# Optimization experiments

Measured on AMD Instinct MI355X. Metric: run time of the kernel, lower is better.

## Reference

```python
import jax, jax.numpy as jnp
import numpy as np

B, S, H = 2, 2048, 1024
NH, DH = 16, 64  # num heads, head dim

def setup_inputs() -> dict:
    key = jax.random.key(0)
    ks = jax.random.split(key, 4)
    scale = 0.02
    return {
        "hidden_states": jax.random.normal(ks[0], (B, S, H), dtype=jnp.float32),
        "attention_mask": jnp.zeros((B, 1, 1, S), dtype=jnp.float32),  # additive mask
        "Wq": jax.random.normal(ks[1], (H, H), dtype=jnp.float32) * scale,
        "bq": jnp.zeros((H,), dtype=jnp.float32),
        "Wk": jax.random.normal(ks[2], (H, H), dtype=jnp.float32) * scale,
        "bk": jnp.zeros((H,), dtype=jnp.float32),
        "Wv": jax.random.normal(ks[3], (H, H), dtype=jnp.float32) * scale,
        "bv": jnp.zeros((H,), dtype=jnp.float32),
    }

def _split_heads(x):
    # [B,S,H] -> [B,NH,S,DH]
    return x.reshape(B, S, NH, DH).transpose(0, 2, 1, 3)

def reference(hidden_states, attention_mask, Wq, bq, Wk, bk, Wv, bv):
    q = _split_heads(hidden_states @ Wq + bq)
    k = _split_heads(hidden_states @ Wk + bk)
    v = _split_heads(hidden_states @ Wv + bv)
    # scores: [B,NH,S,S]
    scores = jnp.einsum('bhqd,bhkd->bhqk', q, k) / jnp.asarray(np.sqrt(DH), scores_dtype := q.dtype)
    scores = scores + attention_mask  # additive mask broadcast
    probs = jax.nn.softmax(scores, axis=-1)
    out = jnp.einsum('bhqk,bhkd->bhqd', probs, v)  # [B,NH,S,DH]
    out = out.transpose(0, 2, 1, 3).reshape(B, S, H)
    return out
```

## Files before the change

### kernel.cpp

```cpp
#include <hip/hip_runtime.h>
#include <hip/hip_bf16.h>

#define Bn  2
#define Sn  2048
#define Hn  1024
#define NHn 16
#define DHn 64
#define Mn  (Bn * Sn)

typedef __attribute__((ext_vector_type(4)))  float    f32x4;
typedef __attribute__((ext_vector_type(16))) float    f32x16;
typedef __attribute__((ext_vector_type(8)))  _Float16 h8;
typedef __attribute__((ext_vector_type(4)))  _Float16 h4;

#define MFMA16F(a, b, c) __builtin_amdgcn_mfma_f32_16x16x32_f16(a, b, c, 0, 0, 0)
#define MFMA32F(a, b, c) __builtin_amdgcn_mfma_f32_32x32x16_f16(a, b, c, 0, 0, 0)

__device__ __forceinline__ void glds16(const void* g, void* l) {
    __builtin_amdgcn_global_load_lds(
        (const __attribute__((address_space(1))) unsigned int*)g,
        (__attribute__((address_space(3))) unsigned int*)l, 16, 0, 0);
}

__global__ __launch_bounds__(256) void cvt_x(
    const float* __restrict__ X, _Float16* __restrict__ Xh)
{
    const int i = blockIdx.x * 256 + threadIdx.x;
    float4 x = ((const float4*)X)[i];
    h4 o;
    o[0] = (_Float16)x.x; o[1] = (_Float16)x.y;
    o[2] = (_Float16)x.z; o[3] = (_Float16)x.w;
    *(h4*)&Xh[(size_t)i * 4] = o;
}

__global__ __launch_bounds__(256) void cvt_wT(
    const float* __restrict__ W0, const float* __restrict__ W1,
    const float* __restrict__ W2, _Float16* __restrict__ WT)
{
    const int which = blockIdx.z;
    const float* W = (which == 0) ? W0 : (which == 1 ? W1 : W2);
    _Float16* O = WT + (size_t)which * Hn * Hn;

    const int k0 = blockIdx.x * 64;
    const int n0 = blockIdx.y * 64;
    const int tid = threadIdx.x;

    __shared__ float Ws[64][65];

#pragma unroll
    for (int it = 0; it < 4; ++it) {
        const int idx = tid + 256 * it;
        const int row = idx >> 4, c4 = (idx & 15) * 4;
        float4 w = *(const float4*)&W[(size_t)(k0 + row) * Hn + n0 + c4];
        Ws[row][c4 + 0] = w.x; Ws[row][c4 + 1] = w.y;
        Ws[row][c4 + 2] = w.z; Ws[row][c4 + 3] = w.w;
    }
    __syncthreads();
#pragma unroll
    for (int it = 0; it < 16; ++it) {
        const int e = tid + 256 * it;
        const int k = e & 63, n = e >> 6;
        O[(size_t)(n0 + n) * Hn + k0 + k] = (_Float16)Ws[k][n];
    }
}

__global__ __launch_bounds__(256) void qkv_mfma(
    const _Float16* __restrict__ Xh, const _Float16* __restrict__ WTA,
    const float* __restrict__ b0, const float* __restrict__ b1,
    const float* __restrict__ b2,
    _Float16* __restrict__ Qh, _Float16* __restrict__ Kh,
    _Float16* __restrict__ VTh)
{
    const int which = blockIdx.z;
    const _Float16* WT = WTA + (size_t)which * Hn * Hn;
    const float* bias = (which == 0) ? b0 : (which == 1 ? b1 : b2);
    _Float16* Dst = (which == 0) ? Qh : (which == 1 ? Kh : VTh);

    const int m0 = blockIdx.x * 128;
    const int n0 = blockIdx.y * 128;
    const int tid  = threadIdx.x;
    const int wid  = tid >> 6;
    const int lane = tid & 63;
    const int l16  = lane & 15;
    const int quad = lane >> 4;
    const int wm = wid >> 1, wn = wid & 1;

    __shared__ _Float16 Ah[128 * 32], Bh[128 * 32];

    f32x4 acc[4][4];
#pragma unroll
    for (int i = 0; i < 4; ++i)
#pragma unroll
        for (int j = 0; j < 4; ++j) acc[i][j] = (f32x4){0.f, 0.f, 0.f, 0.f};

    for (int kt = 0; kt < Hn / 32; ++kt) {
        const int k0 = kt * 32;
        __syncthreads();
#pragma unroll
        for (int c = 0; c < 2; ++c) {
            const int idx = (wid * 2 + c) * 64 + lane;
            const int row = idx >> 2;
            const int cg  = (idx & 3) ^ (row & 3);
            glds16(&Xh[(size_t)(m0 + row) * Hn + k0 + cg * 8],
                   &Ah[(wid * 2 + c) * 512]);
            glds16(&WT[(size_t)(n0 + row) * Hn + k0 + cg * 8],
                   &Bh[(wid * 2 + c) * 512]);
        }
        __syncthreads();

        h8 xa[4], wb[4];
#pragma unroll
        for (int t = 0; t < 4; ++t) {
            const int ar = wm * 64 + t * 16 + l16;
            const int br = wn * 64 + t * 16 + l16;
            xa[t] = *(const h8*)&Ah[ar * 32 + ((quad ^ (ar & 3)) * 8)];
            wb[t] = *(const h8*)&Bh[br * 32 + ((quad ^ (br & 3)) * 8)];
        }
        if (which < 2) {
#pragma unroll
            for (int i = 0; i < 4; ++i)
#pragma unroll
                for (int j = 0; j < 4; ++j)
                    acc[i][j] = MFMA16F(xa[i], wb[j], acc[i][j]);
        } else {
#pragma unroll
            for (int i = 0; i < 4; ++i)
#pragma unroll
                for (int j = 0; j < 4; ++j)
                    acc[i][j] = MFMA16F(wb[i], xa[j], acc[i][j]);
        }
    }

    if (which < 2) {
#pragma unroll
        for (int j = 0; j < 4; ++j) {
            const int n = n0 + wn * 64 + j * 16 + l16;
            const float bv = bias[n];
            const int hh = n >> 6, dd = n & 63;
#pragma unroll
            for (int i = 0; i < 4; ++i) {
                const int mb = m0 + wm * 64 + i * 16 + quad * 4;
#pragma unroll
                for (int r = 0; r < 4; ++r) {
                    const int m = mb + r;
                    const int b = m >> 11, s = m & (Sn - 1);
                    Dst[(((size_t)b * NHn + hh) * Sn + s) * DHn + dd] =
                        (_Float16)(acc[i][j][r] + bv);
                }
            }
        }
    } else {
#pragma unroll
        for (int i = 0; i < 4; ++i) {
#pragma unroll
            for (int r = 0; r < 4; ++r) {
                const int n = n0 + wn * 64 + i * 16 + quad * 4 + r;
                const float bv = bias[n];
                const int hh = n >> 6, dd = n & 63;
#pragma unroll
                for (int j = 0; j < 4; ++j) {
                    const int m = m0 + wm * 64 + j * 16 + l16;
                    const int b = m >> 11, s = m & (Sn - 1);
                    Dst[(((size_t)b * NHn + hh) * DHn + dd) * Sn + s] =
                        (_Float16)(acc[i][j][r] + bv);
                }
            }
        }
    }
}

__global__ __launch_bounds__(256) void attn(
    const _Float16* __restrict__ Qh, const _Float16* __restrict__ Kh,
    const _Float16* __restrict__ VTh, const float* __restrict__ mask,
    float* __restrict__ Out)
{
    const int qb = blockIdx.x;
    const int h  = blockIdx.y;
    const int b  = blockIdx.z;
    const int bh = b * NHn + h;

    const int tid  = threadIdx.x;
    const int wid  = tid >> 6;
    const int lane = tid & 63;
    const int l32  = lane & 31;
    const int hi   = lane >> 5;

    __shared__ _Float16 Kb[2][4096];
    __shared__ _Float16 Vb[2][4096];
    __shared__ _Float16 Pws[4][32 * 72];
    __shared__ float Mlds[2][64];
    __shared__ float Ilds[4][32];

    const int q0 = qb * 128 + wid * 32;
    const size_t qbase = ((size_t)bh * Sn + q0 + l32) * DHn;
    h8 qf[4];
#pragma unroll
    for (int kd = 0; kd < 4; ++kd)
        qf[kd] = *(const h8*)&Qh[qbase + kd * 16 + hi * 8];

    f32x16 o[2];
#pragma unroll
    for (int dt = 0; dt < 2; ++dt) o[dt] = (f32x16)(0.f);
    float l_lane = 0.f;

    const _Float16* Kg = Kh  + (size_t)bh * Sn * DHn;
    const _Float16* Vg = VTh + (size_t)bh * DHn * Sn;

#pragma unroll
    for (int c = 0; c < 2; ++c) {
        const int idx = (wid * 2 + c) * 64 + lane;
        const int row = idx >> 3;
        const int cg  = (idx & 7) ^ (row & 7);
        glds16(&Kg[(size_t)row * DHn + cg * 8], &Kb[0][(wid * 2 + c) * 512]);
        glds16(&Vg[(size_t)row * Sn  + cg * 8], &Vb[0][(wid * 2 + c) * 512]);
    }
    if (tid < 64) Mlds[0][tid] = mask[(size_t)b * Sn + tid];

    for (int kt = 0; kt < Sn / 64; ++kt) {
        const int cur = kt & 1;
        __syncthreads();

        if (kt + 1 < Sn / 64) {
            const int nxt = cur ^ 1;
            const int koff = (kt + 1) * 64;
#pragma unroll
            for (int c = 0; c < 2; ++c) {
                const int idx = (wid * 2 + c) * 64 + lane;
                const int row = idx >> 3;
                const int cg  = (idx & 7) ^ (row & 7);
                glds16(&Kg[(size_t)(koff + row) * DHn + cg * 8],
                       &Kb[nxt][(wid * 2 + c) * 512]);
                glds16(&Vg[(size_t)row * Sn + koff + cg * 8],
                       &Vb[nxt][(wid * 2 + c) * 512]);
            }
            if (tid < 64) Mlds[nxt][tid] = mask[(size_t)b * Sn + koff + tid];
        }

        f32x16 s[2];
#pragma unroll
        for (int t = 0; t < 2; ++t) {
            f32x16 c = (f32x16)(0.f);
#pragma unroll
            for (int kd = 0; kd < 4; ++kd) {
                const int row = t * 32 + l32;
                h8 kf = *(const h8*)&Kb[cur][row * 64 +
                                             (((kd * 2 + hi) ^ (row & 7)) * 8)];
                c = MFMA32F(kf, qf[kd], c);
            }
            s[t] = c;
        }

#pragma unroll
        for (int t = 0; t < 2; ++t) {
#pragma unroll
            for (int g2 = 0; g2 < 4; ++g2) {
                float4 mv = *(const float4*)&Mlds[cur][t * 32 + hi * 4 + g2 * 8];
                h4 pk;
#pragma unroll
                for (int e = 0; e < 4; ++e) {
                    const float p = __expf(s[t][g2 * 4 + e] * 0.125f +
                                           ((const float*)&mv)[e]);
                    l_lane += p;
                    pk[e] = (_Float16)p;
                }
                *(h4*)&Pws[wid][l32 * 72 + t * 32 + hi * 4 + g2 * 8] = pk;
            }
        }

#pragma unroll
        for (int ks = 0; ks < 4; ++ks) {
            h8 pa = *(const h8*)&Pws[wid][l32 * 72 + ks * 16 + hi * 8];
#pragma unroll
            for (int dt = 0; dt < 2; ++dt) {
                const int row = dt * 32 + l32;
                h8 vf = *(const h8*)&Vb[cur][row * 64 +
                                             (((ks * 2 + hi) ^ (row & 7)) * 8)];
                o[dt] = MFMA32F(pa, vf, o[dt]);
            }
        }
    }

    const float l_tot = l_lane + __shfl_xor(l_lane, 32);
    if (lane < 32) Ilds[wid][l32] = 1.0f / l_tot;

#pragma unroll
    for (int g2 = 0; g2 < 4; ++g2) {
        float4 iv = *(const float4*)&Ilds[wid][hi * 4 + g2 * 8];
#pragma unroll
        for (int e = 0; e < 4; ++e) {
            const int r = g2 * 4 + e;
            const int q = q0 + 4 * hi + 8 * g2 + e;
            const size_t ob = ((size_t)b * Sn + q) * Hn + h * DHn;
            const float sc = ((const float*)&iv)[e];
#pragma unroll
            for (int dt = 0; dt < 2; ++dt)
                Out[ob + dt * 32 + l32] = o[dt][r] * sc;
        }
    }
}

extern "C" void kernel_launch(void* const* d_in, const int* in_sizes, int n_in,
                              void* d_out, int out_size, void* d_ws, size_t ws_size,
                              hipStream_t stream) {
    const float* X    = (const float*)d_in[0];
    const float* mask = (const float*)d_in[1];
    const float* Wq   = (const float*)d_in[2];
    const float* bq   = (const float*)d_in[3];
    const float* Wk   = (const float*)d_in[4];
    const float* bk   = (const float*)d_in[5];
    const float* Wv   = (const float*)d_in[6];
    const float* bv   = (const float*)d_in[7];
    float* out = (float*)d_out;

    const size_t NE = (size_t)Mn * Hn;
    _Float16* Xh  = (_Float16*)d_ws;
    _Float16* WT  = Xh + NE;
    _Float16* Qh  = WT + (size_t)3 * Hn * Hn;
    _Float16* Kh  = Qh + NE;
    _Float16* VTh = Kh + NE;

    cvt_x<<<dim3(Mn * Hn / 1024), dim3(256), 0, stream>>>(X, Xh);
    cvt_wT<<<dim3(16, 16, 3), dim3(256), 0, stream>>>(Wq, Wk, Wv, WT);

    dim3 g1(Mn / 128, Hn / 128, 3), b1(256);
    qkv_mfma<<<g1, b1, 0, stream>>>(Xh, WT, bq, bk, bv, Qh, Kh, VTh);

    dim3 g2(Sn / 128, NHn, Bn), b2(256);
    attn<<<g2, b2, 0, stream>>>(Qh, Kh, VTh, mask, out);
}
```

Measured before the change: 190.6 us.

## Triple-buffer K/V, swap LDS P staging for permlane32 swaps, remap block order

The attention kernel moves from double to triple buffering of K/V tiles, using explicit vmcnt waits and raw barriers so loads run two tiles ahead. The probability tile no longer round-trips through LDS; it is rearranged into MFMA operand layout in registers with permlane32_swap. The whole mask row is preloaded once, pre-scaled by log2(e), so exp becomes exp2. Block indices are remapped so neighbouring blocks cover different heads, and s_setprio is raised around the MFMA sections. In exchange the kernel uses more LDS per block and relies on hand-written waitcnt counts being correct.

```diff
diff --git a/kernel.cpp b/kernel.cpp
--- a/kernel.cpp
+++ b/kernel.cpp
@@ -12,6 +12,10 @@
 typedef __attribute__((ext_vector_type(16))) float    f32x16;
 typedef __attribute__((ext_vector_type(8)))  _Float16 h8;
 typedef __attribute__((ext_vector_type(4)))  _Float16 h4;
+typedef __attribute__((ext_vector_type(2)))  unsigned int u32x2;
+
+union H2U  { _Float16 h[2]; unsigned int u; };
+union U4H8 { unsigned int u[4]; h8 v; };
 
 #define MFMA16F(a, b, c) __builtin_amdgcn_mfma_f32_16x16x32_f16(a, b, c, 0, 0, 0)
 #define MFMA32F(a, b, c) __builtin_amdgcn_mfma_f32_32x32x16_f16(a, b, c, 0, 0, 0)
@@ -174,10 +178,10 @@
     const _Float16* __restrict__ VTh, const float* __restrict__ mask,
     float* __restrict__ Out)
 {
-    const int qb = blockIdx.x;
-    const int h  = blockIdx.y;
-    const int b  = blockIdx.z;
-    const int bh = b * NHn + h;
+    const int flat = blockIdx.x + 16 * blockIdx.y + 256 * blockIdx.z;
+    const int bh   = ((flat & 7) << 2) | ((flat >> 3) & 3);
+    const int qb   = flat >> 5;
+    const int b = bh >> 4, h = bh & 15;
 
     const int tid  = threadIdx.x;
     const int wid  = tid >> 6;
@@ -185,58 +189,70 @@
     const int l32  = lane & 31;
     const int hi   = lane >> 5;
 
-    __shared__ _Float16 Kb[2][4096];
-    __shared__ _Float16 Vb[2][4096];
-    __shared__ _Float16 Pws[4][32 * 72];
-    __shared__ float Mlds[2][64];
-    __shared__ float Ilds[4][32];
+    __shared__ __align__(16) _Float16 Kb[3][4096];
+    __shared__ __align__(16) _Float16 Vb[3][4096];
+    __shared__ float4 Ml4[Sn / 4];
+    __shared__ float  Ilds[4][32];
+    const float* Ml = (const float*)Ml4;
 
     const int q0 = qb * 128 + wid * 32;
+
     const size_t qbase = ((size_t)bh * Sn + q0 + l32) * DHn;
     h8 qf[4];
 #pragma unroll
     for (int kd = 0; kd < 4; ++kd)
         qf[kd] = *(const h8*)&Qh[qbase + kd * 16 + hi * 8];
 
+    {
+        const float4* mg = (const float4*)(mask + (size_t)b * Sn);
+        float4 m0 = mg[tid], m1 = mg[tid + 256];
+        const float L2E = 1.44269504088896340736f;
+        float4 a0 = {m0.x * L2E, m0.y * L2E, m0.z * L2E, m0.w * L2E};
+        float4 a1 = {m1.x * L2E, m1.y * L2E, m1.z * L2E, m1.w * L2E};
+        Ml4[tid] = a0;
+        Ml4[tid + 256] = a1;
+    }
+
+    const _Float16* Kg = Kh  + (size_t)bh * Sn * DHn;
+    const _Float16* Vg = VTh + (size_t)bh * DHn * Sn;
+
+    auto stage = [&](int kt, int buf) {
+        const int koff = kt * 64;
+#pragma unroll
+        for (int c = 0; c < 2; ++c) {
+            const int idx = (wid * 2 + c) * 64 + lane;
+            const int row = idx >> 3;
+            const int cg  = (idx & 7) ^ (row & 7);
+            glds16(&Kg[(size_t)(koff + row) * DHn + cg * 8],
+                   &Kb[buf][(wid * 2 + c) * 512]);
+            glds16(&Vg[(size_t)row * Sn + koff + cg * 8],
+                   &Vb[buf][(wid * 2 + c) * 512]);
+        }
+    };
+
+    stage(0, 0);
+    stage(1, 1);
+    asm volatile("s_waitcnt lgkmcnt(0)" ::: "memory");
+
     f32x16 o[2];
 #pragma unroll
     for (int dt = 0; dt < 2; ++dt) o[dt] = (f32x16)(0.f);
     float l_lane = 0.f;
 
-    const _Float16* Kg = Kh  + (size_t)bh * Sn * DHn;
-    const _Float16* Vg = VTh + (size_t)bh * DHn * Sn;
-
-#pragma unroll
-    for (int c = 0; c < 2; ++c) {
-        const int idx = (wid * 2 + c) * 64 + lane;
-        const int row = idx >> 3;
-        const int cg  = (idx & 7) ^ (row & 7);
-        glds16(&Kg[(size_t)row * DHn + cg * 8], &Kb[0][(wid * 2 + c) * 512]);
-        glds16(&Vg[(size_t)row * Sn  + cg * 8], &Vb[0][(wid * 2 + c) * 512]);
-    }
-    if (tid < 64) Mlds[0][tid] = mask[(size_t)b * Sn + tid];
-
+    int cur = 0;
     for (int kt = 0; kt < Sn / 64; ++kt) {
-        const int cur = kt & 1;
-        __syncthreads();
-
-        if (kt + 1 < Sn / 64) {
-            const int nxt = cur ^ 1;
-            const int koff = (kt + 1) * 64;
-#pragma unroll
-            for (int c = 0; c < 2; ++c) {
-                const int idx = (wid * 2 + c) * 64 + lane;
-                const int row = idx >> 3;
-                const int cg  = (idx & 7) ^ (row & 7);
-                glds16(&Kg[(size_t)(koff + row) * DHn + cg * 8],
-                       &Kb[nxt][(wid * 2 + c) * 512]);
-                glds16(&Vg[(size_t)row * Sn + koff + cg * 8],
-                       &Vb[nxt][(wid * 2 + c) * 512]);
-            }
-            if (tid < 64) Mlds[nxt][tid] = mask[(size_t)b * Sn + koff + tid];
+        if (kt < Sn / 64 - 1) asm volatile("s_waitcnt vmcnt(4)" ::: "memory");
+        else                  asm volatile("s_waitcnt vmcnt(0)" ::: "memory");
+        __builtin_amdgcn_s_barrier();
+        asm volatile("" ::: "memory");
+
+        if (kt + 2 < Sn / 64) {
+            int stb = cur - 1; if (stb < 0) stb = 2;
+            stage(kt + 2, stb);
         }
 
         f32x16 s[2];
+        __builtin_amdgcn_s_setprio(1);
 #pragma unroll
         for (int t = 0; t < 2; ++t) {
             f32x16 c = (f32x16)(0.f);
@@ -249,35 +265,48 @@
             }
             s[t] = c;
         }
-
+        __builtin_amdgcn_s_setprio(0);
+
+        const float SC = 0.18033688011112042f;
+        unsigned int pk[2][4][2];
 #pragma unroll
         for (int t = 0; t < 2; ++t) {
 #pragma unroll
-            for (int g2 = 0; g2 < 4; ++g2) {
-                float4 mv = *(const float4*)&Mlds[cur][t * 32 + hi * 4 + g2 * 8];
-                h4 pk;
-#pragma unroll
-                for (int e = 0; e < 4; ++e) {
-                    const float p = __expf(s[t][g2 * 4 + e] * 0.125f +
-                                           ((const float*)&mv)[e]);
-                    l_lane += p;
-                    pk[e] = (_Float16)p;
-                }
-                *(h4*)&Pws[wid][l32 * 72 + t * 32 + hi * 4 + g2 * 8] = pk;
-            }
-        }
-
+            for (int g = 0; g < 4; ++g) {
+                float4 mv = *(const float4*)&Ml[kt * 64 + t * 32 + hi * 4 + g * 8];
+                const float p0 = __builtin_amdgcn_exp2f(s[t][g * 4 + 0] * SC + mv.x);
+                const float p1 = __builtin_amdgcn_exp2f(s[t][g * 4 + 1] * SC + mv.y);
+                const float p2 = __builtin_amdgcn_exp2f(s[t][g * 4 + 2] * SC + mv.z);
+                const float p3 = __builtin_amdgcn_exp2f(s[t][g * 4 + 3] * SC + mv.w);
+                l_lane += (p0 + p1) + (p2 + p3);
+                H2U a, c2;
+                a.h[0]  = (_Float16)p0; a.h[1]  = (_Float16)p1;
+                c2.h[0] = (_Float16)p2; c2.h[1] = (_Float16)p3;
+                pk[t][g][0] = a.u; pk[t][g][1] = c2.u;
+            }
+        }
+
+        __builtin_amdgcn_s_setprio(1);
 #pragma unroll
         for (int ks = 0; ks < 4; ++ks) {
-            h8 pa = *(const h8*)&Pws[wid][l32 * 72 + ks * 16 + hi * 8];
+            const int t = ks >> 1, ge = (ks & 1) * 2;
+            u32x2 rA = __builtin_amdgcn_permlane32_swap(
+                pk[t][ge][0], pk[t][ge + 1][0], false, false);
+            u32x2 rB = __builtin_amdgcn_permlane32_swap(
+                pk[t][ge][1], pk[t][ge + 1][1], false, false);
+            U4H8 w;
+            w.u[0] = rA[0]; w.u[1] = rB[0]; w.u[2] = rA[1]; w.u[3] = rB[1];
 #pragma unroll
             for (int dt = 0; dt < 2; ++dt) {
                 const int row = dt * 32 + l32;
                 h8 vf = *(const h8*)&Vb[cur][row * 64 +
                                              (((ks * 2 + hi) ^ (row & 7)) * 8)];
-                o[dt] = MFMA32F(pa, vf, o[dt]);
-            }
-        }
+                o[dt] = MFMA32F(w.v, vf, o[dt]);
+            }
+        }
+        __builtin_amdgcn_s_setprio(0);
+
+        cur = (cur == 2) ? 0 : cur + 1;
     }
 
     const float l_tot = l_lane + __shfl_xor(l_lane, 32);
```

Result: faster. 184.2 us (-3.4%).
